# Performance work log

Measured on AMD Instinct MI355X. Metric: run time of the kernel, lower is better.

## Reference

```python
import jax, jax.numpy as jnp
import numpy as np

# Config (matches init_kwargs)
L, B, D, V = 12, 8, 2048, 32000
H, HD, G, N, K = 64, 64, 8, 128, 4
I = H * HD                 # intermediate_size = 4096
CONV = I + 2 * G * N       # conv_dim = 6144
P = I + CONV + H           # in_proj output = 10304
TMAX = 10000.0             # finite replacement for inf time_step_limit


def rmsnorm(x, w, eps=1e-5):
    x32 = x.astype(jnp.float32)
    return (x32 * jax.lax.rsqrt(jnp.mean(x32 * x32, axis=-1, keepdims=True) + eps)) * w


def setup_inputs() -> dict:
    key = jax.random.key(0)
    ks = jax.random.split(key, 10)
    s = 0.02
    return {
        "input_ids": jax.random.randint(ks[0], (B, 1), 0, V),
        "conv_states": jax.random.normal(ks[1], (L, B, CONV, K), dtype=jnp.float32),
        "ssm_states": jax.random.normal(ks[2], (L, B, H, HD, N), dtype=jnp.float32) * 0.1,
        "emb": jax.random.normal(ks[3], (V, D), dtype=jnp.float32) * s,
        "norm_w": jnp.ones((L, D), jnp.float32),
        "in_proj_w": jax.random.normal(ks[4], (L, D, P), dtype=jnp.float32) * s,
        "conv_w": jax.random.normal(ks[5], (L, CONV, K), dtype=jnp.float32) * s,
        "conv_b": jnp.zeros((L, CONV), jnp.float32),
        "dt_bias": jax.random.normal(ks[6], (L, H), dtype=jnp.float32) * s,
        "A_log": jnp.log(jnp.broadcast_to(jnp.arange(1, H + 1, dtype=jnp.float32), (L, H))),
        "D_param": jnp.ones((L, H), jnp.float32),
        "gn_w": jnp.ones((L, I), jnp.float32),
        "out_proj_w": jax.random.normal(ks[7], (L, I, D), dtype=jnp.float32) * s,
        "norm_f_w": jnp.ones((D,), jnp.float32),
        "lm_head_w": jax.random.normal(ks[8], (V, D), dtype=jnp.float32) * s,
    }


def reference(input_ids, conv_states, ssm_states, emb, norm_w, in_proj_w, conv_w,
              conv_b, dt_bias, A_log, D_param, gn_w, out_proj_w, norm_f_w, lm_head_w):
    h = emb[input_ids]  # [B,1,D]

    def layer(h, xs):
        cs, ss, nw, wi, cw, cb, db, al, dp, gw, wo = xs
        residual = h
        hn = rmsnorm(h, nw)                                   # block.norm (RMSNorm)
        proj = jnp.einsum('btd,dp->btp', hn, wi)              # in_proj
        gate, hBC, dt = jnp.split(proj, [I, I + CONV], axis=-1)
        # conv state shift + depthwise conv over kernel dim
        new_in = hBC[:, 0, :]                                 # [B, CONV]
        new_cs = jnp.concatenate([cs[:, :, 1:], new_in[:, :, None]], axis=-1)  # [B,CONV,K]
        conv_out = jnp.sum(new_cs * cw[None], axis=-1) + cb
        conv_out = jax.nn.silu(conv_out)
        x, Bv, Cv = jnp.split(conv_out, [I, I + G * N], axis=-1)
        x = x.reshape(B, H, HD)
        # dt: softplus(dt + dt_bias), clamp to [0, 10000]
        dt_ = jax.nn.softplus(dt[:, 0, :] + db[None, :])       # [B,H]
        dt_ = jnp.clip(dt_, 0.0, TMAX)
        A = -jnp.exp(al)                                       # [H], fp32
        dA = jnp.exp(dt_[:, :, None, None] * A[None, :, None, None])  # [B,H,1,1]
        rep = H // G
        Brep = jnp.repeat(Bv.reshape(B, G, N), rep, axis=1)    # [B,H,N]
        Crep = jnp.repeat(Cv.reshape(B, G, N), rep, axis=1)
        dBx = dt_[:, :, None, None] * Brep[:, :, None, :] * x[:, :, :, None]  # [B,H,HD,N]
        new_ss = ss * dA + dBx
        y = jnp.sum(new_ss * Crep[:, :, None, :], axis=-1)     # [B,H,HD]
        y = y + x * dp[None, :, None]                          # skip via D
        y = y.reshape(B, 1, I)
        # gated RMSNorm: (y * silu(gate)) -> rmsnorm * weight
        yg = y.astype(jnp.float32) * jax.nn.silu(gate.astype(jnp.float32))
        y = rmsnorm(yg, gw)
        out = jnp.einsum('bti,id->btd', y, wo)                 # out_proj
        return residual + out, (new_cs, new_ss)

    h, (new_conv, new_ssm) = jax.lax.scan(
        layer, h,
        (conv_states, ssm_states, norm_w, in_proj_w, conv_w, conv_b,
         dt_bias, A_log, D_param, gn_w, out_proj_w))
    hf = rmsnorm(h, norm_f_w)                                  # norm_f
    logits = jnp.einsum('btd,vd->btv', hf, lm_head_w).astype(jnp.float32)
    return logits, new_conv, new_ssm
```

## Files before the change

### kernel.cpp

```cpp
#include <hip/hip_runtime.h>
#include <hip/hip_bf16.h>
#include <math.h>

#define LNUM 12
#define BNUM 8
#define DNUM 2048
#define VNUM 32000
#define HNUM 64
#define HDNUM 64
#define GNUM 8
#define NNUM 128
#define KNUM 4
#define INUM (HNUM*HDNUM)
#define CONVNUM (INUM + 2*GNUM*NNUM)
#define PNUM (INUM + CONVNUM + HNUM)

#define IP_KC 16
#define GRID 1024

struct MParams {
  const int* ids;
  const float* conv_states; const float* ssm_states;
  const float* emb; const float* norm_w; const float* in_proj_w;
  const float* conv_w; const float* conv_b; const float* dt_bias;
  const float* A_log; const float* D_param; const float* gn_w;
  const float* out_proj_w;
  float* conv_out_st; float* ssm_out_st;
  float* h; float* yg; float* ygsq; float* sqp; float* part1;
  int* arrive;
  int* release;
};

__device__ __forceinline__ float sigmoidf_(float x){ return 1.f/(1.f+expf(-x)); }

__device__ __forceinline__ int   uc_load_i (const int* p){ return __hip_atomic_load((int*)p, __ATOMIC_RELAXED, __HIP_MEMORY_SCOPE_AGENT); }
__device__ __forceinline__ void  uc_store_i(int* p, int v){ __hip_atomic_store(p, v, __ATOMIC_RELAXED, __HIP_MEMORY_SCOPE_AGENT); }
__device__ __forceinline__ float uc_load_f (const float* p){ return __hip_atomic_load((float*)p, __ATOMIC_RELAXED, __HIP_MEMORY_SCOPE_AGENT); }
__device__ __forceinline__ void  uc_store_f(float* p, float v){ __hip_atomic_store(p, v, __ATOMIC_RELAXED, __HIP_MEMORY_SCOPE_AGENT); }
__device__ __forceinline__ void  uc_add_f  (float* p, float v){ __hip_atomic_fetch_add(p, v, __ATOMIC_RELAXED, __HIP_MEMORY_SCOPE_AGENT); }

__device__ __forceinline__ void gbar(const MParams& P, int epoch){
  __syncthreads();
  if (blockIdx.x == 0){
    for (int i = 1 + threadIdx.x; i < GRID; i += 256){
      long spins = 0;
      while (uc_load_i(&P.arrive[i*16]) < epoch){
        __builtin_amdgcn_s_sleep(1);
        if (++spins > (1L<<22)) break;
      }
    }
    __syncthreads();
    if (threadIdx.x == 0){
      asm volatile("s_waitcnt vmcnt(0) lgkmcnt(0)" ::: "memory");
      uc_store_i(P.release, epoch);
    }
  } else {
    if (threadIdx.x == 0){
      asm volatile("s_waitcnt vmcnt(0) lgkmcnt(0)" ::: "memory");
      uc_store_i(&P.arrive[blockIdx.x*16], epoch);
      long spins = 0;
      while (uc_load_i(P.release) < epoch){
        __builtin_amdgcn_s_sleep(1);
        if (++spins > (1L<<22)) break;
      }
    }
    __syncthreads();
  }
  asm volatile("" ::: "memory");
}

__global__ __launch_bounds__(256, 4) void k_mamba(MParams P){
  const int blk = blockIdx.x, t = threadIdx.x;
  const int w = t >> 6, l = t & 63;
  __shared__ float smem[3088];
  int bar_no = 0;

  if (blk < BNUM){
    int b = blk;
    const float* src = P.emb + (size_t)P.ids[b]*DNUM;
    float* dst = P.h + (size_t)b*DNUM;
    float4 v0 = *(const float4*)(src + t*4);
    float4 v1 = *(const float4*)(src + 1024 + t*4);
    uc_store_f(dst + t*4 + 0, v0.x); uc_store_f(dst + t*4 + 1, v0.y);
    uc_store_f(dst + t*4 + 2, v0.z); uc_store_f(dst + t*4 + 3, v0.w);
    uc_store_f(dst + 1024 + t*4 + 0, v1.x); uc_store_f(dst + 1024 + t*4 + 1, v1.y);
    uc_store_f(dst + 1024 + t*4 + 2, v1.z); uc_store_f(dst + 1024 + t*4 + 3, v1.w);
    float q = v0.x*v0.x+v0.y*v0.y+v0.z*v0.z+v0.w*v0.w
            + v1.x*v1.x+v1.y*v1.y+v1.z*v1.z+v1.w*v1.w;
    q += __shfl_xor(q,32); q += __shfl_xor(q,16); q += __shfl_xor(q,8);
    q += __shfl_xor(q,4);  q += __shfl_xor(q,2);  q += __shfl_xor(q,1);
    if (l == 0) smem[w] = q;
    __syncthreads();
    if (t == 0) uc_store_f(&P.sqp[b], smem[0]+smem[1]+smem[2]+smem[3]);
  }
  gbar(P, ++bar_no);

  for (int li = 0; li < LNUM; ++li){
    const float* Wi   = P.in_proj_w  + (size_t)li*DNUM*PNUM;
    const float* nw   = P.norm_w     + (size_t)li*DNUM;
    const float* cw   = P.conv_w     + (size_t)li*CONVNUM*KNUM;
    const float* cb   = P.conv_b     + (size_t)li*CONVNUM;
    const float* db   = P.dt_bias    + (size_t)li*HNUM;
    const float* al   = P.A_log      + (size_t)li*HNUM;
    const float* dpp  = P.D_param    + (size_t)li*HNUM;
    const float* gw   = P.gn_w       + (size_t)li*INUM;
    const float* Wo   = P.out_proj_w + (size_t)li*INUM*DNUM;
    const float* csin = P.conv_states + (size_t)li*BNUM*CONVNUM*KNUM;
    float*       csout= P.conv_out_st + (size_t)li*BNUM*CONVNUM*KNUM;
    const float* ssin = P.ssm_states  + (size_t)li*BNUM*HNUM*HDNUM*NNUM;
    float*       ssout= P.ssm_out_st  + (size_t)li*BNUM*HNUM*HDNUM*NNUM;

    {
      float*  xs  = smem;
      float4* red = (float4*)(smem + 1024);
      if (blk < 896){
        int pb = blk % 56, kc = blk / 56;
        int r0 = kc*128;
        for (int i = t; i < BNUM*128; i += 256){
          int b = i>>7, dl = i&127;
          xs[i] = uc_load_f(&P.h[b*DNUM + r0 + dl]) * nw[r0 + dl];
        }
        __syncthreads();
        int p0 = pb*256 + l*4;
        bool valid = (p0 < PNUM);
        float4 acc[BNUM];
        #pragma unroll
        for (int b = 0; b < BNUM; ++b) acc[b] = make_float4(0.f,0.f,0.f,0.f);
        if (valid){
          int rbase = w*32;
          const float* wp = Wi + (size_t)(r0 + rbase)*PNUM + p0;
          #pragma unroll 4
          for (int r = 0; r < 32; ++r){
            float4 w4 = *(const float4*)wp;
            wp += PNUM;
            #pragma unroll
            for (int b = 0; b < BNUM; ++b){
              float xvv = xs[b*128 + rbase + r];
              acc[b].x += xvv*w4.x; acc[b].y += xvv*w4.y; acc[b].z += xvv*w4.z; acc[b].w += xvv*w4.w;
            }
          }
        }
        #pragma unroll
        for (int rw = 1; rw < 4; ++rw){
          if (w == rw){
            #pragma unroll
            for (int b = 0; b < BNUM; ++b) red[b*64 + l] = acc[b];
          }
          __syncthreads();
          if (w == 0){
            #pragma unroll
            for (int b = 0; b < BNUM; ++b){
              float4 r4 = red[b*64 + l];
              acc[b].x += r4.x; acc[b].y += r4.y; acc[b].z += r4.z; acc[b].w += r4.w;
            }
          }
          __syncthreads();
        }
        if (w == 0){
          #pragma unroll
          for (int b = 0; b < BNUM; ++b) red[b*64 + l] = acc[b];
        }
        __syncthreads();
        const float* redf = (const float*)red;
        if (pb*256 + t < PNUM){
          #pragma unroll
          for (int b = 0; b < BNUM; ++b)
            uc_store_f(&P.part1[(size_t)(kc*BNUM + b)*PNUM + pb*256 + t], redf[b*256 + t]);
        }
      } else if (blk < 896 + BNUM){
        int b = blk - 896;
        float q = 0.f;
        for (int i = t; i < DNUM; i += 256){
          float v = uc_load_f(&P.h[b*DNUM + i]);
          q += v*v;
        }
        q += __shfl_xor(q,32); q += __shfl_xor(q,16); q += __shfl_xor(q,8);
        q += __shfl_xor(q,4);  q += __shfl_xor(q,2);  q += __shfl_xor(q,1);
        if (l == 0) smem[w] = q;
        __syncthreads();
        if (t == 0) uc_store_f(&P.sqp[b], smem[0]+smem[1]+smem[2]+smem[3]);
      }
    }
    gbar(P, ++bar_no);

    {
      float* xv    = smem;
      float* gatel = smem + 32;
      float* Bsh   = smem + 64;
      float* Csh   = smem + 192;
      float* scal  = smem + 320;
      float* sred  = smem + 328;
      int b = blk >> 7, rest = blk & 127, hh = rest >> 1, half = rest & 1, g = hh >> 3;
      if (t == 0) scal[2] = rsqrtf(uc_load_f(&P.sqp[b]) * (1.f/DNUM) + 1e-5f);
      __syncthreads();
      float inv = scal[2];
      {
        int n = t & 127;
        int c = (t < 128) ? (INUM + g*NNUM + n) : (INUM + GNUM*NNUM + g*NNUM + n);
        int p = INUM + c;
        float v = 0.f;
        #pragma unroll
        for (int kc2 = 0; kc2 < IP_KC; ++kc2) v += uc_load_f(&P.part1[(size_t)(kc2*BNUM + b)*PNUM + p]);
        v *= inv;
        size_t sid = (size_t)b*CONVNUM + c;
        float4 s4 = *(const float4*)(csin + sid*KNUM);
        float4 ns = make_float4(s4.y, s4.z, s4.w, v);
        if ((hh & 7) == 0 && half == 0) *(float4*)(csout + sid*KNUM) = ns;
        float4 w4 = *(const float4*)(cw + (size_t)c*KNUM);
        float co = ns.x*w4.x + ns.y*w4.y + ns.z*w4.z + ns.w*w4.w + cb[c];
        float sv = co * sigmoidf_(co);
        if (t < 128) Bsh[n] = sv; else Csh[n] = sv;
      }
      if (t < 32){
        int hd = half*32 + t;
        int c = hh*HDNUM + hd;
        int p = INUM + c;
        float v = 0.f;
        #pragma unroll
        for (int kc2 = 0; kc2 < IP_KC; ++kc2) v += uc_load_f(&P.part1[(size_t)(kc2*BNUM + b)*PNUM + p]);
        v *= inv;
        size_t sid = (size_t)b*CONVNUM + c;
        float4 s4 = *(const float4*)(csin + sid*KNUM);
        float4 ns = make_float4(s4.y, s4.z, s4.w, v);
        *(float4*)(csout + sid*KNUM) = ns;
        float4 w4 = *(const float4*)(cw + (size_t)c*KNUM);
        float co = ns.x*w4.x + ns.y*w4.y + ns.z*w4.z + ns.w*w4.w + cb[c];
        xv[t] = co * sigmoidf_(co);
      } else if (t < 64){
        int hd = half*32 + (t-32);
        int p = hh*HDNUM + hd;
        float v = 0.f;
        #pragma unroll
        for (int kc2 = 0; kc2 < IP_KC; ++kc2) v += uc_load_f(&P.part1[(size_t)(kc2*BNUM + b)*PNUM + p]);
        gatel[t-32] = v * inv;
      } else if (t == 64){
        int p = INUM + CONVNUM + hh;
        float v = 0.f;
        #pragma unroll
        for (int kc2 = 0; kc2 < IP_KC; ++kc2) v += uc_load_f(&P.part1[(size_t)(kc2*BNUM + b)*PNUM + p]);
        float dtr = v*inv + db[hh];
        float dt = (dtr > 20.f) ? dtr : log1pf(expf(dtr));
        dt = fminf(dt, 10000.f);
        scal[0] = dt;
        scal[1] = expf(dt * (-expf(al[hh])));
      }
      __syncthreads();
      float dt = scal[0], dA = scal[1], dp = dpp[hh];
      int r = t & 31, a2 = t >> 5;
      float4 Bv = *(float4*)&Bsh[r*4];
      float4 Cv = *(float4*)&Csh[r*4];
      const float* si = ssin  + (size_t)(b*HNUM + hh)*HDNUM*NNUM + half*4096;
      float*       so = ssout + (size_t)(b*HNUM + hh)*HDNUM*NNUM + half*4096;
      float s_yg = 0.f;
      #pragma unroll
      for (int k = 0; k < 4; ++k){
        int hdl = k*8 + a2;
        float xvv = xv[hdl];
        float coef = dt * xvv;
        int off = k*1024 + t*4;
        float4 s4 = *(const float4*)(si + off);
        float4 ns;
        ns.x = s4.x*dA + coef*Bv.x;
        ns.y = s4.y*dA + coef*Bv.y;
        ns.z = s4.z*dA + coef*Bv.z;
        ns.w = s4.w*dA + coef*Bv.w;
        *(float4*)(so + off) = ns;
        float yp = ns.x*Cv.x + ns.y*Cv.y + ns.z*Cv.z + ns.w*Cv.w;
        yp += __shfl_xor(yp,1); yp += __shfl_xor(yp,2); yp += __shfl_xor(yp,4);
        yp += __shfl_xor(yp,8); yp += __shfl_xor(yp,16);
        if (r == 0){
          float gv = gatel[hdl];
          float ygv = (yp + xvv*dp) * gv * sigmoidf_(gv);
          uc_store_f(&P.yg[b*INUM + hh*HDNUM + half*32 + hdl], ygv);
          s_yg += ygv*ygv;
        }
      }
      if (r == 0) sred[a2] = s_yg;
      __syncthreads();
      if (t == 0){
        float tot = 0.f;
        #pragma unroll
        for (int j = 0; j < 8; ++j) tot += sred[j];
        uc_store_f(&P.ygsq[b*128 + hh*2 + half], tot);
      }
    }
    gbar(P, ++bar_no);

    {
      float*  xs   = smem;
      float*  invg = smem + 512;
      float2* red2 = (float2*)(smem + 528);
      int pb = blk & 15, kc = blk >> 4;
      if (t < 64){
        int b2 = t>>3, j = t&7;
        float v = 0.f;
        #pragma unroll
        for (int jj = 0; jj < 16; ++jj) v += uc_load_f(&P.ygsq[b2*128 + j + jj*8]);
        v += __shfl_xor(v,1); v += __shfl_xor(v,2); v += __shfl_xor(v,4);
        if (j == 0) invg[b2] = rsqrtf(v*(1.f/INUM) + 1e-5f);
      }
      __syncthreads();
      int r0 = kc*64;
      for (int i = t; i < BNUM*64; i += 256){
        int b = i>>6, il = i&63;
        xs[i] = uc_load_f(&P.yg[b*INUM + r0 + il]) * invg[b] * gw[r0 + il];
      }
      __syncthreads();
      int c0 = pb*128 + l*2;
      float2 acc[BNUM];
      #pragma unroll
      for (int b = 0; b < BNUM; ++b) acc[b] = make_float2(0.f,0.f);
      {
        int rbase = w*16;
        const float* wp = Wo + (size_t)(r0 + rbase)*DNUM + c0;
        #pragma unroll 4
        for (int r2 = 0; r2 < 16; ++r2){
          float2 w2 = *(const float2*)wp;
          wp += DNUM;
          #pragma unroll
          for (int b = 0; b < BNUM; ++b){
            float xvv = xs[b*64 + rbase + r2];
            acc[b].x += xvv*w2.x; acc[b].y += xvv*w2.y;
          }
        }
      }
      #pragma unroll
      for (int rw = 1; rw < 4; ++rw){
        if (w == rw){
          #pragma unroll
          for (int b = 0; b < BNUM; ++b) red2[b*64 + l] = acc[b];
        }
        __syncthreads();
        if (w == 0){
          #pragma unroll
          for (int b = 0; b < BNUM; ++b){
            float2 r2v = red2[b*64 + l];
            acc[b].x += r2v.x; acc[b].y += r2v.y;
          }
        }
        __syncthreads();
      }
      if (w == 0){
        #pragma unroll
        for (int b = 0; b < BNUM; ++b) red2[b*64 + l] = acc[b];
      }
      __syncthreads();
      const float* redf = (const float*)red2;
      #pragma unroll
      for (int bb = 0; bb < 4; ++bb){
        int b = bb*2 + (t>>7);
        int cc = t & 127;
        uc_add_f(&P.h[b*DNUM + pb*128 + cc], redf[b*128 + cc]);
      }
    }
    gbar(P, ++bar_no);
  }

  if (blk >= 896 && blk < 896 + BNUM){
    int b = blk - 896;
    float q = 0.f;
    for (int i = t; i < DNUM; i += 256){
      float v = uc_load_f(&P.h[b*DNUM + i]);
      q += v*v;
    }
    q += __shfl_xor(q,32); q += __shfl_xor(q,16); q += __shfl_xor(q,8);
    q += __shfl_xor(q,4);  q += __shfl_xor(q,2);  q += __shfl_xor(q,1);
    if (l == 0) smem[w] = q;
    __syncthreads();
    if (t == 0) uc_store_f(&P.sqp[b], smem[0]+smem[1]+smem[2]+smem[3]);
  }
}

__global__ __launch_bounds__(256) void k_lmhead(const float* __restrict__ h,
                                                const float* __restrict__ sqp,
                                                const float* __restrict__ nf,
                                                const float* __restrict__ Wl,
                                                float* __restrict__ logits){
  __shared__ float hs[BNUM*DNUM];
  __shared__ float invb_s[8];
  int t = threadIdx.x;
  if (t < 8) invb_s[t] = rsqrtf(sqp[t]*(1.f/DNUM) + 1e-5f);
  __syncthreads();
  #pragma unroll
  for (int it = 0; it < 16; ++it){
    int i = t*4 + it*1024;
    float iv = invb_s[it>>1];
    float4 hv  = *(const float4*)(h + i);
    float4 nfv = *(const float4*)(nf + (i & 2047));
    float4 o;
    o.x = hv.x*iv*nfv.x; o.y = hv.y*iv*nfv.y; o.z = hv.z*iv*nfv.z; o.w = hv.w*iv*nfv.w;
    *(float4*)(hs + i) = o;
  }
  __syncthreads();
  int wv = t >> 6, lane = t & 63;
  int v0 = (blockIdx.x*4 + wv)*4;
  float acc[4][BNUM];
  #pragma unroll
  for (int u = 0; u < 4; ++u)
    #pragma unroll
    for (int b = 0; b < BNUM; ++b) acc[u][b] = 0.f;
  #pragma unroll
  for (int j = 0; j < 8; ++j){
    int dbase = j*256 + lane*4;
    float4 w0 = *(const float4*)(Wl + (size_t)(v0+0)*DNUM + dbase);
    float4 w1 = *(const float4*)(Wl + (size_t)(v0+1)*DNUM + dbase);
    float4 w2 = *(const float4*)(Wl + (size_t)(v0+2)*DNUM + dbase);
    float4 w3 = *(const float4*)(Wl + (size_t)(v0+3)*DNUM + dbase);
    #pragma unroll
    for (int b = 0; b < BNUM; ++b){
      float4 hv = *(const float4*)(hs + b*DNUM + dbase);
      acc[0][b] += w0.x*hv.x + w0.y*hv.y + w0.z*hv.z + w0.w*hv.w;
      acc[1][b] += w1.x*hv.x + w1.y*hv.y + w1.z*hv.z + w1.w*hv.w;
      acc[2][b] += w2.x*hv.x + w2.y*hv.y + w2.z*hv.z + w2.w*hv.w;
      acc[3][b] += w3.x*hv.x + w3.y*hv.y + w3.z*hv.z + w3.w*hv.w;
    }
  }
  #pragma unroll
  for (int u = 0; u < 4; ++u)
    #pragma unroll
    for (int b = 0; b < BNUM; ++b){
      float s = acc[u][b];
      s += __shfl_xor(s,32); s += __shfl_xor(s,16); s += __shfl_xor(s,8);
      s += __shfl_xor(s,4);  s += __shfl_xor(s,2);  s += __shfl_xor(s,1);
      if (lane == 0) logits[(size_t)b*VNUM + v0 + u] = s;
    }
}

extern "C" void kernel_launch(void* const* d_in, const int* in_sizes, int n_in,
                              void* d_out, int out_size, void* d_ws, size_t ws_size,
                              hipStream_t stream){
  const int*   ids         = (const int*)d_in[0];
  const float* conv_states = (const float*)d_in[1];
  const float* ssm_states  = (const float*)d_in[2];
  const float* emb         = (const float*)d_in[3];
  const float* norm_w      = (const float*)d_in[4];
  const float* in_proj_w   = (const float*)d_in[5];
  const float* conv_w      = (const float*)d_in[6];
  const float* conv_b      = (const float*)d_in[7];
  const float* dt_bias     = (const float*)d_in[8];
  const float* A_log       = (const float*)d_in[9];
  const float* D_param     = (const float*)d_in[10];
  const float* gn_w        = (const float*)d_in[11];
  const float* out_proj_w  = (const float*)d_in[12];
  const float* norm_f_w    = (const float*)d_in[13];
  const float* lm_head_w   = (const float*)d_in[14];

  float* out         = (float*)d_out;
  float* logits      = out;
  float* conv_out_st = out + (size_t)BNUM*VNUM;
  float* ssm_out_st  = conv_out_st + (size_t)LNUM*BNUM*CONVNUM*KNUM;

  float* ws    = (float*)d_ws;
  float* h     = ws;
  float* yg    = h    + 16384;
  float* ygsq  = yg   + 32768;
  float* sqp   = ygsq + 1024;
  float* part1 = sqp  + 64;
  int*   bar   = (int*)(part1 + 1830912);

  hipMemsetAsync(bar, 0, (GRID*16 + 16)*sizeof(int), stream);

  MParams P;
  P.ids = ids; P.conv_states = conv_states; P.ssm_states = ssm_states;
  P.emb = emb; P.norm_w = norm_w; P.in_proj_w = in_proj_w;
  P.conv_w = conv_w; P.conv_b = conv_b; P.dt_bias = dt_bias;
  P.A_log = A_log; P.D_param = D_param; P.gn_w = gn_w;
  P.out_proj_w = out_proj_w;
  P.conv_out_st = conv_out_st; P.ssm_out_st = ssm_out_st;
  P.h = h; P.yg = yg; P.ygsq = ygsq; P.sqp = sqp; P.part1 = part1;
  P.arrive = bar; P.release = bar + GRID*16;

  k_mamba<<<GRID, 256, 0, stream>>>(P);
  k_lmhead<<<VNUM/16, 256, 0, stream>>>(h, sqp, norm_f_w, lm_head_w, logits);
}
```

Baseline: 1.155 ms.

## Replace global barriers with per-stage dataflow counters and retile out_proj

Replaces the centralized grid barrier with per-stage counter flags. The SSM stage now waits only on the in_proj column strips and the norm partial it needs, and out_proj waits on grouped completion counters. The in_proj grid is trimmed to 41 strips × 16 K-chunks. out_proj is retiled to 512-row K-chunks with 16-column strips and a different shared-memory reduction. The aim is to cut barrier latency and idle time between stages, at the cost of more flag traffic, larger shared memory, and correctness that depends on the flag counts and timeouts.

Result: slower. 1.381 ms (+19.5%).

```diff
diff --git a/kernel.cpp b/kernel.cpp
--- a/kernel.cpp
+++ b/kernel.cpp
@@ -16,6 +16,8 @@
 #define PNUM (INUM + CONVNUM + HNUM)
 
 #define IP_KC 16
+#define NSTRIP 41
+#define A_TILES (NSTRIP*IP_KC)
 #define GRID 1024
 
 struct MParams {
@@ -27,53 +29,59 @@
   const float* out_proj_w;
   float* conv_out_st; float* ssm_out_st;
   float* h; float* yg; float* ygsq; float* sqp; float* part1;
-  int* arrive;
-  int* release;
+  int* flagE; int* flagS; int* flagA; int* flagC; int* flagD;
 };
 
 __device__ __forceinline__ float sigmoidf_(float x){ return 1.f/(1.f+expf(-x)); }
 
 __device__ __forceinline__ int   uc_load_i (const int* p){ return __hip_atomic_load((int*)p, __ATOMIC_RELAXED, __HIP_MEMORY_SCOPE_AGENT); }
-__device__ __forceinline__ void  uc_store_i(int* p, int v){ __hip_atomic_store(p, v, __ATOMIC_RELAXED, __HIP_MEMORY_SCOPE_AGENT); }
 __device__ __forceinline__ float uc_load_f (const float* p){ return __hip_atomic_load((float*)p, __ATOMIC_RELAXED, __HIP_MEMORY_SCOPE_AGENT); }
 __device__ __forceinline__ void  uc_store_f(float* p, float v){ __hip_atomic_store(p, v, __ATOMIC_RELAXED, __HIP_MEMORY_SCOPE_AGENT); }
 __device__ __forceinline__ void  uc_add_f  (float* p, float v){ __hip_atomic_fetch_add(p, v, __ATOMIC_RELAXED, __HIP_MEMORY_SCOPE_AGENT); }
-
-__device__ __forceinline__ void gbar(const MParams& P, int epoch){
+__device__ __forceinline__ void  uc_inc_i  (int* p){ __hip_atomic_fetch_add(p, 1, __ATOMIC_RELAXED, __HIP_MEMORY_SCOPE_AGENT); }
+
+__device__ __forceinline__ void flag_inc(int* line){
   __syncthreads();
-  if (blockIdx.x == 0){
-    for (int i = 1 + threadIdx.x; i < GRID; i += 256){
-      long spins = 0;
-      while (uc_load_i(&P.arrive[i*16]) < epoch){
-        __builtin_amdgcn_s_sleep(1);
-        if (++spins > (1L<<22)) break;
-      }
+  if (threadIdx.x == 0){
+    asm volatile("s_waitcnt vmcnt(0) lgkmcnt(0)" ::: "memory");
+    uc_inc_i(line);
+  }
+}
+
+__device__ __forceinline__ void wait_line(const int* line, int target){
+  if (threadIdx.x == 0){
+    long sp = 0;
+    while (uc_load_i(line) < target){
+      __builtin_amdgcn_s_sleep(4);
+      if (++sp > (1L<<19)) break;
+    }
+  }
+  __syncthreads();
+}
+
+__device__ __forceinline__ void wait_grp(const int* grp, int target){
+  __shared__ int done_s;
+  if (threadIdx.x == 0) done_s = 0;
+  __syncthreads();
+  long sp = 0;
+  for (;;){
+    if (threadIdx.x < 64){
+      int v = (threadIdx.x < 32) ? uc_load_i(&grp[threadIdx.x*16]) : 0;
+      v += __shfl_xor(v,1); v += __shfl_xor(v,2); v += __shfl_xor(v,4);
+      v += __shfl_xor(v,8); v += __shfl_xor(v,16); v += __shfl_xor(v,32);
+      if (threadIdx.x == 0) done_s = (v >= target);
     }
     __syncthreads();
-    if (threadIdx.x == 0){
-      asm volatile("s_waitcnt vmcnt(0) lgkmcnt(0)" ::: "memory");
-      uc_store_i(P.release, epoch);
-    }
-  } else {
-    if (threadIdx.x == 0){
-      asm volatile("s_waitcnt vmcnt(0) lgkmcnt(0)" ::: "memory");
-      uc_store_i(&P.arrive[blockIdx.x*16], epoch);
-      long spins = 0;
-      while (uc_load_i(P.release) < epoch){
-        __builtin_amdgcn_s_sleep(1);
-        if (++spins > (1L<<22)) break;
-      }
-    }
+    if (done_s || ++sp > (1L<<18)) break;
+    __builtin_amdgcn_s_sleep(4);
     __syncthreads();
   }
-  asm volatile("" ::: "memory");
 }
 
 __global__ __launch_bounds__(256, 4) void k_mamba(MParams P){
   const int blk = blockIdx.x, t = threadIdx.x;
   const int w = t >> 6, l = t & 63;
-  __shared__ float smem[3088];
-  int bar_no = 0;
+  __shared__ float smem[8256];
 
   if (blk < BNUM){
     int b = blk;
@@ -85,15 +93,8 @@
     uc_store_f(dst + t*4 + 2, v0.z); uc_store_f(dst + t*4 + 3, v0.w);
     uc_store_f(dst + 1024 + t*4 + 0, v1.x); uc_store_f(dst + 1024 + t*4 + 1, v1.y);
     uc_store_f(dst + 1024 + t*4 + 2, v1.z); uc_store_f(dst + 1024 + t*4 + 3, v1.w);
-    float q = v0.x*v0.x+v0.y*v0.y+v0.z*v0.z+v0.w*v0.w
-            + v1.x*v1.x+v1.y*v1.y+v1.z*v1.z+v1.w*v1.w;
-    q += __shfl_xor(q,32); q += __shfl_xor(q,16); q += __shfl_xor(q,8);
-    q += __shfl_xor(q,4);  q += __shfl_xor(q,2);  q += __shfl_xor(q,1);
-    if (l == 0) smem[w] = q;
-    __syncthreads();
-    if (t == 0) uc_store_f(&P.sqp[b], smem[0]+smem[1]+smem[2]+smem[3]);
-  }
-  gbar(P, ++bar_no);
+    flag_inc(P.flagE);
+  }
 
   for (int li = 0; li < LNUM; ++li){
     const float* Wi   = P.in_proj_w  + (size_t)li*DNUM*PNUM;
@@ -110,87 +111,111 @@
     const float* ssin = P.ssm_states  + (size_t)li*BNUM*HNUM*HDNUM*NNUM;
     float*       ssout= P.ssm_out_st  + (size_t)li*BNUM*HNUM*HDNUM*NNUM;
 
-    {
+    if (li == 0) wait_line(P.flagE, BNUM);
+    else         wait_grp(P.flagD + (li-1)*512, GRID);
+
+    if (blk < A_TILES){
       float*  xs  = smem;
-      float4* red = (float4*)(smem + 1024);
-      if (blk < 896){
-        int pb = blk % 56, kc = blk / 56;
-        int r0 = kc*128;
-        for (int i = t; i < BNUM*128; i += 256){
-          int b = i>>7, dl = i&127;
-          xs[i] = uc_load_f(&P.h[b*DNUM + r0 + dl]) * nw[r0 + dl];
+      float4* red = (float4*)(smem + 1040);
+      int pb = blk % NSTRIP, kc = blk / NSTRIP;
+      int r0 = kc*128;
+      for (int i = t; i < BNUM*128; i += 256){
+        int b = i>>7, dl = i&127;
+        xs[i] = uc_load_f(&P.h[b*DNUM + r0 + dl]) * nw[r0 + dl];
+      }
+      __syncthreads();
+      int p0 = pb*256 + l*4;
+      bool valid = (p0 < PNUM);
+      float4 acc[BNUM];
+      #pragma unroll
+      for (int b = 0; b < BNUM; ++b) acc[b] = make_float4(0.f,0.f,0.f,0.f);
+      if (valid){
+        int rbase = w*32;
+        const float* wp = Wi + (size_t)(r0 + rbase)*PNUM + p0;
+        #pragma unroll 4
+        for (int r = 0; r < 32; ++r){
+          float4 w4 = *(const float4*)wp;
+          wp += PNUM;
+          #pragma unroll
+          for (int b = 0; b < BNUM; ++b){
+            float xvv = xs[b*128 + rbase + r];
+            acc[b].x += xvv*w4.x; acc[b].y += xvv*w4.y; acc[b].z += xvv*w4.z; acc[b].w += xvv*w4.w;
+          }
+        }
+      }
+      #pragma unroll
+      for (int rw = 1; rw < 4; ++rw){
+        if (w == rw){
+          #pragma unroll
+          for (int b = 0; b < BNUM; ++b) red[b*64 + l] = acc[b];
         }
         __syncthreads();
-        int p0 = pb*256 + l*4;
-        bool valid = (p0 < PNUM);
-        float4 acc[BNUM];
-        #pragma unroll
-        for (int b = 0; b < BNUM; ++b) acc[b] = make_float4(0.f,0.f,0.f,0.f);
-        if (valid){
-          int rbase = w*32;
-          const float* wp = Wi + (size_t)(r0 + rbase)*PNUM + p0;
-          #pragma unroll 4
-          for (int r = 0; r < 32; ++r){
-            float4 w4 = *(const float4*)wp;
-            wp += PNUM;
-            #pragma unroll
-            for (int b = 0; b < BNUM; ++b){
-              float xvv = xs[b*128 + rbase + r];
-              acc[b].x += xvv*w4.x; acc[b].y += xvv*w4.y; acc[b].z += xvv*w4.z; acc[b].w += xvv*w4.w;
-            }
-          }
-        }
-        #pragma unroll
-        for (int rw = 1; rw < 4; ++rw){
-          if (w == rw){
-            #pragma unroll
-            for (int b = 0; b < BNUM; ++b) red[b*64 + l] = acc[b];
-          }
-          __syncthreads();
-          if (w == 0){
-            #pragma unroll
-            for (int b = 0; b < BNUM; ++b){
-              float4 r4 = red[b*64 + l];
-              acc[b].x += r4.x; acc[b].y += r4.y; acc[b].z += r4.z; acc[b].w += r4.w;
-            }
-          }
-          __syncthreads();
-        }
         if (w == 0){
           #pragma unroll
-          for (int b = 0; b < BNUM; ++b) red[b*64 + l] = acc[b];
+          for (int b = 0; b < BNUM; ++b){
+            float4 r4 = red[b*64 + l];
+            acc[b].x += r4.x; acc[b].y += r4.y; acc[b].z += r4.z; acc[b].w += r4.w;
+          }
         }
         __syncthreads();
-        const float* redf = (const float*)red;
-        if (pb*256 + t < PNUM){
-          #pragma unroll
-          for (int b = 0; b < BNUM; ++b)
-            uc_store_f(&P.part1[(size_t)(kc*BNUM + b)*PNUM + pb*256 + t], redf[b*256 + t]);
-        }
-      } else if (blk < 896 + BNUM){
-        int b = blk - 896;
-        float q = 0.f;
-        for (int i = t; i < DNUM; i += 256){
-          float v = uc_load_f(&P.h[b*DNUM + i]);
-          q += v*v;
-        }
-        q += __shfl_xor(q,32); q += __shfl_xor(q,16); q += __shfl_xor(q,8);
-        q += __shfl_xor(q,4);  q += __shfl_xor(q,2);  q += __shfl_xor(q,1);
-        if (l == 0) smem[w] = q;
+      }
+      if (w == 0){
+        #pragma unroll
+        for (int b = 0; b < BNUM; ++b) red[b*64 + l] = acc[b];
+      }
+      __syncthreads();
+      const float* redf = (const float*)red;
+      if (pb*256 + t < PNUM){
+        #pragma unroll
+        for (int b = 0; b < BNUM; ++b)
+          uc_store_f(&P.part1[(size_t)(kc*BNUM + b)*PNUM + pb*256 + t], redf[b*256 + t]);
+      }
+      flag_inc(&P.flagA[li*896 + pb*16]);
+    } else if (blk < A_TILES + BNUM){
+      int b = blk - A_TILES;
+      float q = 0.f;
+      for (int i = t; i < DNUM; i += 256){
+        float v = uc_load_f(&P.h[b*DNUM + i]);
+        q += v*v;
+      }
+      q += __shfl_xor(q,32); q += __shfl_xor(q,16); q += __shfl_xor(q,8);
+      q += __shfl_xor(q,4);  q += __shfl_xor(q,2);  q += __shfl_xor(q,1);
+      if (l == 0) smem[w] = q;
+      __syncthreads();
+      if (t == 0) uc_store_f(&P.sqp[b], smem[0]+smem[1]+smem[2]+smem[3]);
+      flag_inc(&P.flagS[li*16]);
+    }
+
+    {
+      int b = blk >> 7, rest = blk & 127, hh = rest >> 1, half = rest & 1, g = hh >> 3;
+      {
+        int s_g = (hh*HDNUM + half*32) >> 8;
+        int s_x = (INUM + hh*HDNUM + half*32) >> 8;
+        int s_B = (2*INUM + g*NNUM) >> 8;
+        int s_C = (2*INUM + GNUM*NNUM + g*NNUM) >> 8;
+        int s_dt = (INUM + CONVNUM) >> 8;
+        const int* line = nullptr; int tgt = IP_KC;
+        if      (t == 0) line = &P.flagA[li*896 + s_g*16];
+        else if (t == 1) line = &P.flagA[li*896 + s_x*16];
+        else if (t == 2) line = &P.flagA[li*896 + s_B*16];
+        else if (t == 3) line = &P.flagA[li*896 + s_C*16];
+        else if (t == 4) line = &P.flagA[li*896 + s_dt*16];
+        else if (t == 5){ line = &P.flagS[li*16]; tgt = BNUM; }
+        if (line){
+          long sp = 0;
+          while (uc_load_i(line) < tgt){
+            __builtin_amdgcn_s_sleep(4);
+            if (++sp > (1L<<19)) break;
+          }
+        }
         __syncthreads();
-        if (t == 0) uc_store_f(&P.sqp[b], smem[0]+smem[1]+smem[2]+smem[3]);
-      }
-    }
-    gbar(P, ++bar_no);
-
-    {
+      }
       float* xv    = smem;
       float* gatel = smem + 32;
       float* Bsh   = smem + 64;
       float* Csh   = smem + 192;
       float* scal  = smem + 320;
       float* sred  = smem + 328;
-      int b = blk >> 7, rest = blk & 127, hh = rest >> 1, half = rest & 1, g = hh >> 3;
       if (t == 0) scal[2] = rsqrtf(uc_load_f(&P.sqp[b]) * (1.f/DNUM) + 1e-5f);
       __syncthreads();
       float inv = scal[2];
@@ -283,14 +308,16 @@
         for (int j = 0; j < 8; ++j) tot += sred[j];
         uc_store_f(&P.ygsq[b*128 + hh*2 + half], tot);
       }
-    }
-    gbar(P, ++bar_no);
+      flag_inc(&P.flagC[li*512 + (blk>>5)*16]);
+    }
 
     {
+      wait_grp(P.flagC + li*512, GRID);
       float*  xs   = smem;
-      float*  invg = smem + 512;
-      float2* red2 = (float2*)(smem + 528);
-      int pb = blk & 15, kc = blk >> 4;
+      float*  invg = smem + 4096;
+      float2* red2 = (float2*)(smem + 4112);
+      int pb = blk & 127, kc = blk >> 7;
+      int c0 = pb*16, r0 = kc*512;
       if (t < 64){
         int b2 = t>>3, j = t&7;
         float v = 0.f;
@@ -300,64 +327,48 @@
         if (j == 0) invg[b2] = rsqrtf(v*(1.f/INUM) + 1e-5f);
       }
       __syncthreads();
-      int r0 = kc*64;
-      for (int i = t; i < BNUM*64; i += 256){
-        int b = i>>6, il = i&63;
+      for (int i = t; i < BNUM*512; i += 256){
+        int b = i>>9, il = i&511;
         xs[i] = uc_load_f(&P.yg[b*INUM + r0 + il]) * invg[b] * gw[r0 + il];
       }
       __syncthreads();
-      int c0 = pb*128 + l*2;
-      float2 acc[BNUM];
+      int cp = t & 7, rg = t >> 3;
+      float2 acc2[BNUM];
       #pragma unroll
-      for (int b = 0; b < BNUM; ++b) acc[b] = make_float2(0.f,0.f);
-      {
-        int rbase = w*16;
-        const float* wp = Wo + (size_t)(r0 + rbase)*DNUM + c0;
-        #pragma unroll 4
-        for (int r2 = 0; r2 < 16; ++r2){
-          float2 w2 = *(const float2*)wp;
-          wp += DNUM;
-          #pragma unroll
-          for (int b = 0; b < BNUM; ++b){
-            float xvv = xs[b*64 + rbase + r2];
-            acc[b].x += xvv*w2.x; acc[b].y += xvv*w2.y;
-          }
+      for (int b = 0; b < BNUM; ++b) acc2[b] = make_float2(0.f,0.f);
+      const float* wp = Wo + (size_t)(r0 + rg)*DNUM + c0 + cp*2;
+      #pragma unroll 4
+      for (int it = 0; it < 16; ++it){
+        float2 w2 = *(const float2*)wp;
+        wp += (size_t)32*DNUM;
+        int rr = rg + it*32;
+        #pragma unroll
+        for (int b = 0; b < BNUM; ++b){
+          float xvv = xs[b*512 + rr];
+          acc2[b].x += xvv*w2.x; acc2[b].y += xvv*w2.y;
         }
       }
       #pragma unroll
-      for (int rw = 1; rw < 4; ++rw){
-        if (w == rw){
-          #pragma unroll
-          for (int b = 0; b < BNUM; ++b) red2[b*64 + l] = acc[b];
-        }
-        __syncthreads();
-        if (w == 0){
-          #pragma unroll
-          for (int b = 0; b < BNUM; ++b){
-            float2 r2v = red2[b*64 + l];
-            acc[b].x += r2v.x; acc[b].y += r2v.y;
-          }
-        }
-        __syncthreads();
-      }
-      if (w == 0){
-        #pragma unroll
-        for (int b = 0; b < BNUM; ++b) red2[b*64 + l] = acc[b];
-      }
-      __syncthreads();
-      const float* redf = (const float*)red2;
-      #pragma unroll
-      for (int bb = 0; bb < 4; ++bb){
-        int b = bb*2 + (t>>7);
-        int cc = t & 127;
-        uc_add_f(&P.h[b*DNUM + pb*128 + cc], redf[b*128 + cc]);
-      }
-    }
-    gbar(P, ++bar_no);
-  }
-
-  if (blk >= 896 && blk < 896 + BNUM){
-    int b = blk - 896;
+      for (int b = 0; b < BNUM; ++b) red2[(rg*8 + cp)*8 + b] = acc2[b];
+      __syncthreads();
+      if (t < 64){
+        int cpi = t & 7, b = t >> 3;
+        float sx = 0.f, sy = 0.f;
+        #pragma unroll 8
+        for (int rgi = 0; rgi < 32; ++rgi){
+          float2 v2 = red2[(rgi*8 + cpi)*8 + b];
+          sx += v2.x; sy += v2.y;
+        }
+        uc_add_f(&P.h[b*DNUM + c0 + cpi*2 + 0], sx);
+        uc_add_f(&P.h[b*DNUM + c0 + cpi*2 + 1], sy);
+      }
+      flag_inc(&P.flagD[li*512 + (blk>>5)*16]);
+    }
+  }
+
+  if (blk >= A_TILES && blk < A_TILES + BNUM){
+    wait_grp(P.flagD + (LNUM-1)*512, GRID);
+    int b = blk - A_TILES;
     float q = 0.f;
     for (int i = t; i < DNUM; i += 256){
       float v = uc_load_f(&P.h[b*DNUM + i]);
@@ -456,9 +467,15 @@
   float* ygsq  = yg   + 32768;
   float* sqp   = ygsq + 1024;
   float* part1 = sqp  + 64;
-  int*   bar   = (int*)(part1 + 1830912);
-
-  hipMemsetAsync(bar, 0, (GRID*16 + 16)*sizeof(int), stream);
+  int*   bar   = (int*)(part1 + 1318912);
+
+  int* flagE = bar;
+  int* flagS = flagE + 16;
+  int* flagA = flagS + 12*16;
+  int* flagC = flagA + 12*56*16;
+  int* flagD = flagC + 12*32*16;
+  size_t flag_bytes = (size_t)(16 + 12*16 + 12*56*16 + 12*32*16 + 12*32*16) * sizeof(int);
+  hipMemsetAsync(bar, 0, flag_bytes, stream);
 
   MParams P;
   P.ids = ids; P.conv_states = conv_states; P.ssm_states = ssm_states;
@@ -468,7 +485,7 @@
   P.out_proj_w = out_proj_w;
   P.conv_out_st = conv_out_st; P.ssm_out_st = ssm_out_st;
   P.h = h; P.yg = yg; P.ygsq = ygsq; P.sqp = sqp; P.part1 = part1;
-  P.arrive = bar; P.release = bar + GRID*16;
+  P.flagE = flagE; P.flagS = flagS; P.flagA = flagA; P.flagC = flagC; P.flagD = flagD;
 
   k_mamba<<<GRID, 256, 0, stream>>>(P);
   k_lmhead<<<VNUM/16, 256, 0, stream>>>(h, sqp, norm_f_w, lm_head_w, logits);
```

## Replace per-phase grid barriers with fine-grained dataflow flags and deferred residual

Applied to the files above, without the earlier changes.

Three of the four grid-wide barriers per layer are replaced with per-strip, per-head and zeroing counters. Consumer blocks poll only the producer tiles they depend on. The out_proj partials now accumulate into a delta buffer, and the gated-RMSNorm scale is folded into the next layer's in_proj input (h_prev + inv*delta) using double-buffered h/delta/ygsq. This removes the separate gated-norm inverse pass before out_proj and lets stages overlap. The in_proj tiling shrinks to 41 strips x 16 k-chunks so the grid tiles are assigned exactly, and unroll factors are raised. The cost is more flag traffic, polling with bounded spins, and more complex correctness ordering.

New measurement: 1.165 ms. About the same (+0.8%).

```diff
diff --git a/kernel.cpp b/kernel.cpp
--- a/kernel.cpp
+++ b/kernel.cpp
@@ -16,6 +16,8 @@
 #define PNUM (INUM + CONVNUM + HNUM)
 
 #define IP_KC 16
+#define NSTRIP 41
+#define A_TILES (NSTRIP*IP_KC)
 #define GRID 1024
 
 struct MParams {
@@ -26,9 +28,10 @@
   const float* A_log; const float* D_param; const float* gn_w;
   const float* out_proj_w;
   float* conv_out_st; float* ssm_out_st;
-  float* h; float* yg; float* ygsq; float* sqp; float* part1;
-  int* arrive;
-  int* release;
+  float* hb0; float* hb1; float* dl0; float* dl1; float* hf;
+  float* yg; float* ygsq; float* sqp; float* part1;
+  int* arrive; int* release;
+  int* flagE; int* flagS; int* flagA; int* flagC; int* flagZ;
 };
 
 __device__ __forceinline__ float sigmoidf_(float x){ return 1.f/(1.f+expf(-x)); }
@@ -38,15 +41,36 @@
 __device__ __forceinline__ float uc_load_f (const float* p){ return __hip_atomic_load((float*)p, __ATOMIC_RELAXED, __HIP_MEMORY_SCOPE_AGENT); }
 __device__ __forceinline__ void  uc_store_f(float* p, float v){ __hip_atomic_store(p, v, __ATOMIC_RELAXED, __HIP_MEMORY_SCOPE_AGENT); }
 __device__ __forceinline__ void  uc_add_f  (float* p, float v){ __hip_atomic_fetch_add(p, v, __ATOMIC_RELAXED, __HIP_MEMORY_SCOPE_AGENT); }
+__device__ __forceinline__ void  uc_inc_i  (int* p){ __hip_atomic_fetch_add(p, 1, __ATOMIC_RELAXED, __HIP_MEMORY_SCOPE_AGENT); }
+
+__device__ __forceinline__ void flag_inc(int* line){
+  __syncthreads();
+  if (threadIdx.x == 0){
+    asm volatile("s_waitcnt vmcnt(0) lgkmcnt(0)" ::: "memory");
+    uc_inc_i(line);
+  }
+}
+
+__device__ __forceinline__ void poll_line(const int* line, int target){
+  long sp = 0;
+  while (uc_load_i(line) < target){
+    __builtin_amdgcn_s_sleep(4);
+    if (++sp > (1L<<20)) break;
+  }
+}
+__device__ __forceinline__ void wait_line(const int* line, int target){
+  if (threadIdx.x == 0) poll_line(line, target);
+  __syncthreads();
+}
 
 __device__ __forceinline__ void gbar(const MParams& P, int epoch){
   __syncthreads();
   if (blockIdx.x == 0){
     for (int i = 1 + threadIdx.x; i < GRID; i += 256){
-      long spins = 0;
+      long sp = 0;
       while (uc_load_i(&P.arrive[i*16]) < epoch){
         __builtin_amdgcn_s_sleep(1);
-        if (++spins > (1L<<22)) break;
+        if (++sp > (1L<<22)) break;
       }
     }
     __syncthreads();
@@ -58,10 +82,10 @@
     if (threadIdx.x == 0){
       asm volatile("s_waitcnt vmcnt(0) lgkmcnt(0)" ::: "memory");
       uc_store_i(&P.arrive[blockIdx.x*16], epoch);
-      long spins = 0;
+      long sp = 0;
       while (uc_load_i(P.release) < epoch){
         __builtin_amdgcn_s_sleep(1);
-        if (++spins > (1L<<22)) break;
+        if (++sp > (1L<<22)) break;
       }
     }
     __syncthreads();
@@ -73,27 +97,20 @@
   const int blk = blockIdx.x, t = threadIdx.x;
   const int w = t >> 6, l = t & 63;
   __shared__ float smem[3088];
-  int bar_no = 0;
+  int ep = 0;
 
   if (blk < BNUM){
     int b = blk;
     const float* src = P.emb + (size_t)P.ids[b]*DNUM;
-    float* dst = P.h + (size_t)b*DNUM;
+    float* dst = P.hb0 + (size_t)b*DNUM;
     float4 v0 = *(const float4*)(src + t*4);
     float4 v1 = *(const float4*)(src + 1024 + t*4);
     uc_store_f(dst + t*4 + 0, v0.x); uc_store_f(dst + t*4 + 1, v0.y);
     uc_store_f(dst + t*4 + 2, v0.z); uc_store_f(dst + t*4 + 3, v0.w);
     uc_store_f(dst + 1024 + t*4 + 0, v1.x); uc_store_f(dst + 1024 + t*4 + 1, v1.y);
     uc_store_f(dst + 1024 + t*4 + 2, v1.z); uc_store_f(dst + 1024 + t*4 + 3, v1.w);
-    float q = v0.x*v0.x+v0.y*v0.y+v0.z*v0.z+v0.w*v0.w
-            + v1.x*v1.x+v1.y*v1.y+v1.z*v1.z+v1.w*v1.w;
-    q += __shfl_xor(q,32); q += __shfl_xor(q,16); q += __shfl_xor(q,8);
-    q += __shfl_xor(q,4);  q += __shfl_xor(q,2);  q += __shfl_xor(q,1);
-    if (l == 0) smem[w] = q;
-    __syncthreads();
-    if (t == 0) uc_store_f(&P.sqp[b], smem[0]+smem[1]+smem[2]+smem[3]);
-  }
-  gbar(P, ++bar_no);
+    flag_inc(P.flagE);
+  }
 
   for (int li = 0; li < LNUM; ++li){
     const float* Wi   = P.in_proj_w  + (size_t)li*DNUM*PNUM;
@@ -110,87 +127,149 @@
     const float* ssin = P.ssm_states  + (size_t)li*BNUM*HNUM*HDNUM*NNUM;
     float*       ssout= P.ssm_out_st  + (size_t)li*BNUM*HNUM*HDNUM*NNUM;
 
-    {
-      float*  xs  = smem;
-      float4* red = (float4*)(smem + 1024);
-      if (blk < 896){
-        int pb = blk % 56, kc = blk / 56;
-        int r0 = kc*128;
+    float* hbase = ((li-1)&1) ? P.hb1 : P.hb0;
+    float* hwrite= (li&1) ? P.hb1 : P.hb0;
+    float* dprev = ((li-1)&1) ? P.dl1 : P.dl0;
+    float* dcur  = (li&1) ? P.dl1 : P.dl0;
+    const float* ygsq_prev = P.ygsq + (((li-1)&1) ? 1024 : 0);
+    float*       ygsq_cur  = P.ygsq + ((li&1) ? 1024 : 0);
+    if (li == 0) hbase = P.hb0;
+
+    if (li == 0) wait_line(P.flagE, BNUM);
+    else         gbar(P, ++ep);
+
+    if (blk < A_TILES){
+      float*  xs   = smem;
+      float*  invs = smem + 1024;
+      float4* red  = (float4*)(smem + 1040);
+      int pb = blk % NSTRIP, kc = blk / NSTRIP;
+      int r0 = kc*128;
+      if (li > 0){
+        if (t < 64){
+          int b2 = t>>3, j = t&7;
+          float v = 0.f;
+          #pragma unroll
+          for (int jj = 0; jj < 16; ++jj) v += uc_load_f(&ygsq_prev[b2*128 + j + jj*8]);
+          v += __shfl_xor(v,1); v += __shfl_xor(v,2); v += __shfl_xor(v,4);
+          if (j == 0) invs[b2] = rsqrtf(v*(1.f/INUM) + 1e-5f);
+        }
+        __syncthreads();
         for (int i = t; i < BNUM*128; i += 256){
           int b = i>>7, dl = i&127;
-          xs[i] = uc_load_f(&P.h[b*DNUM + r0 + dl]) * nw[r0 + dl];
-        }
-        __syncthreads();
-        int p0 = pb*256 + l*4;
-        bool valid = (p0 < PNUM);
-        float4 acc[BNUM];
-        #pragma unroll
-        for (int b = 0; b < BNUM; ++b) acc[b] = make_float4(0.f,0.f,0.f,0.f);
-        if (valid){
-          int rbase = w*32;
-          const float* wp = Wi + (size_t)(r0 + rbase)*PNUM + p0;
-          #pragma unroll 4
-          for (int r = 0; r < 32; ++r){
-            float4 w4 = *(const float4*)wp;
-            wp += PNUM;
-            #pragma unroll
-            for (int b = 0; b < BNUM; ++b){
-              float xvv = xs[b*128 + rbase + r];
-              acc[b].x += xvv*w4.x; acc[b].y += xvv*w4.y; acc[b].z += xvv*w4.z; acc[b].w += xvv*w4.w;
-            }
+          float hv = uc_load_f(&hbase[b*DNUM + r0 + dl]) + invs[b]*uc_load_f(&dprev[b*DNUM + r0 + dl]);
+          xs[i] = hv * nw[r0 + dl];
+        }
+      } else {
+        for (int i = t; i < BNUM*128; i += 256){
+          int b = i>>7, dl = i&127;
+          xs[i] = uc_load_f(&hbase[b*DNUM + r0 + dl]) * nw[r0 + dl];
+        }
+      }
+      __syncthreads();
+      int p0 = pb*256 + l*4;
+      bool valid = (p0 < PNUM);
+      float4 acc[BNUM];
+      #pragma unroll
+      for (int b = 0; b < BNUM; ++b) acc[b] = make_float4(0.f,0.f,0.f,0.f);
+      if (valid){
+        int rbase = w*32;
+        const float* wp = Wi + (size_t)(r0 + rbase)*PNUM + p0;
+        #pragma unroll 8
+        for (int r = 0; r < 32; ++r){
+          float4 w4 = *(const float4*)wp;
+          wp += PNUM;
+          #pragma unroll
+          for (int b = 0; b < BNUM; ++b){
+            float xvv = xs[b*128 + rbase + r];
+            acc[b].x += xvv*w4.x; acc[b].y += xvv*w4.y; acc[b].z += xvv*w4.z; acc[b].w += xvv*w4.w;
           }
         }
-        #pragma unroll
-        for (int rw = 1; rw < 4; ++rw){
-          if (w == rw){
-            #pragma unroll
-            for (int b = 0; b < BNUM; ++b) red[b*64 + l] = acc[b];
+      }
+      #pragma unroll
+      for (int rw = 1; rw < 4; ++rw){
+        if (w == rw){
+          #pragma unroll
+          for (int b = 0; b < BNUM; ++b) red[b*64 + l] = acc[b];
+        }
+        __syncthreads();
+        if (w == 0){
+          #pragma unroll
+          for (int b = 0; b < BNUM; ++b){
+            float4 r4 = red[b*64 + l];
+            acc[b].x += r4.x; acc[b].y += r4.y; acc[b].z += r4.z; acc[b].w += r4.w;
           }
-          __syncthreads();
-          if (w == 0){
-            #pragma unroll
-            for (int b = 0; b < BNUM; ++b){
-              float4 r4 = red[b*64 + l];
-              acc[b].x += r4.x; acc[b].y += r4.y; acc[b].z += r4.z; acc[b].w += r4.w;
-            }
-          }
-          __syncthreads();
-        }
-        if (w == 0){
-          #pragma unroll
-          for (int b = 0; b < BNUM; ++b) red[b*64 + l] = acc[b];
-        }
-        __syncthreads();
-        const float* redf = (const float*)red;
-        if (pb*256 + t < PNUM){
-          #pragma unroll
-          for (int b = 0; b < BNUM; ++b)
-            uc_store_f(&P.part1[(size_t)(kc*BNUM + b)*PNUM + pb*256 + t], redf[b*256 + t]);
-        }
-      } else if (blk < 896 + BNUM){
-        int b = blk - 896;
-        float q = 0.f;
-        for (int i = t; i < DNUM; i += 256){
-          float v = uc_load_f(&P.h[b*DNUM + i]);
-          q += v*v;
-        }
-        q += __shfl_xor(q,32); q += __shfl_xor(q,16); q += __shfl_xor(q,8);
-        q += __shfl_xor(q,4);  q += __shfl_xor(q,2);  q += __shfl_xor(q,1);
-        if (l == 0) smem[w] = q;
-        __syncthreads();
-        if (t == 0) uc_store_f(&P.sqp[b], smem[0]+smem[1]+smem[2]+smem[3]);
-      }
-    }
-    gbar(P, ++bar_no);
+        }
+        __syncthreads();
+      }
+      if (w == 0){
+        #pragma unroll
+        for (int b = 0; b < BNUM; ++b) red[b*64 + l] = acc[b];
+      }
+      __syncthreads();
+      const float* redf = (const float*)red;
+      if (pb*256 + t < PNUM){
+        #pragma unroll
+        for (int b = 0; b < BNUM; ++b)
+          uc_store_f(&P.part1[(size_t)(kc*BNUM + b)*PNUM + pb*256 + t], redf[b*256 + t]);
+      }
+      flag_inc(&P.flagA[(li*NSTRIP + pb)*16]);
+    } else if (blk < A_TILES + BNUM){
+      int b = blk - A_TILES;
+      float ivg = 0.f;
+      if (li > 0){
+        float v = (t < 128) ? uc_load_f(&ygsq_prev[b*128 + t]) : 0.f;
+        v += __shfl_xor(v,1); v += __shfl_xor(v,2); v += __shfl_xor(v,4);
+        v += __shfl_xor(v,8); v += __shfl_xor(v,16); v += __shfl_xor(v,32);
+        if (l == 0) smem[w] = v;
+        __syncthreads();
+        ivg = rsqrtf((smem[0]+smem[1]+smem[2]+smem[3])*(1.f/INUM) + 1e-5f);
+        __syncthreads();
+      }
+      float q = 0.f;
+      for (int i = t; i < DNUM; i += 256){
+        float hv;
+        if (li > 0){
+          hv = uc_load_f(&hbase[b*DNUM + i]) + ivg*uc_load_f(&dprev[b*DNUM + i]);
+          uc_store_f(&hwrite[b*DNUM + i], hv);
+        } else {
+          hv = uc_load_f(&hbase[b*DNUM + i]);
+        }
+        q += hv*hv;
+      }
+      q += __shfl_xor(q,32); q += __shfl_xor(q,16); q += __shfl_xor(q,8);
+      q += __shfl_xor(q,4);  q += __shfl_xor(q,2);  q += __shfl_xor(q,1);
+      if (l == 0) smem[4+w] = q;
+      __syncthreads();
+      if (t == 0) uc_store_f(&P.sqp[b], smem[4]+smem[5]+smem[6]+smem[7]);
+      flag_inc(&P.flagS[li*16]);
+    } else if (blk < A_TILES + BNUM + 16){
+      int z = blk - A_TILES - BNUM;
+      for (int i = t; i < 1024; i += 256) uc_store_f(&dcur[z*1024 + i], 0.f);
+      flag_inc(&P.flagZ[li*16]);
+    }
 
     {
+      int b = blk >> 7, rest = blk & 127, hh = rest >> 1, half = rest & 1, g = hh >> 3;
+      {
+        int s_g  = (hh*HDNUM + half*32) >> 8;
+        int s_x  = (INUM + hh*HDNUM + half*32) >> 8;
+        int s_B  = (2*INUM + g*NNUM) >> 8;
+        int s_C  = (2*INUM + GNUM*NNUM + g*NNUM) >> 8;
+        int s_dt = (INUM + CONVNUM) >> 8;
+        if      (t == 0) poll_line(&P.flagA[(li*NSTRIP + s_g)*16], IP_KC);
+        else if (t == 1) poll_line(&P.flagA[(li*NSTRIP + s_x)*16], IP_KC);
+        else if (t == 2) poll_line(&P.flagA[(li*NSTRIP + s_B)*16], IP_KC);
+        else if (t == 3) poll_line(&P.flagA[(li*NSTRIP + s_C)*16], IP_KC);
+        else if (t == 4) poll_line(&P.flagA[(li*NSTRIP + s_dt)*16], IP_KC);
+        else if (t == 5) poll_line(&P.flagS[li*16], BNUM);
+        __syncthreads();
+      }
       float* xv    = smem;
       float* gatel = smem + 32;
       float* Bsh   = smem + 64;
       float* Csh   = smem + 192;
       float* scal  = smem + 320;
       float* sred  = smem + 328;
-      int b = blk >> 7, rest = blk & 127, hh = rest >> 1, half = rest & 1, g = hh >> 3;
       if (t == 0) scal[2] = rsqrtf(uc_load_f(&P.sqp[b]) * (1.f/DNUM) + 1e-5f);
       __syncthreads();
       float inv = scal[2];
@@ -281,29 +360,22 @@
         float tot = 0.f;
         #pragma unroll
         for (int j = 0; j < 8; ++j) tot += sred[j];
-        uc_store_f(&P.ygsq[b*128 + hh*2 + half], tot);
-      }
-    }
-    gbar(P, ++bar_no);
+        uc_store_f(&ygsq_cur[b*128 + hh*2 + half], tot);
+      }
+      flag_inc(&P.flagC[(li*HNUM + hh)*16]);
+    }
 
     {
+      int pb = blk & 15, kc = blk >> 4;
+      if      (t == 0) poll_line(&P.flagC[(li*HNUM + kc)*16], 16);
+      else if (t == 1) poll_line(&P.flagZ[li*16], 16);
+      __syncthreads();
       float*  xs   = smem;
-      float*  invg = smem + 512;
       float2* red2 = (float2*)(smem + 528);
-      int pb = blk & 15, kc = blk >> 4;
-      if (t < 64){
-        int b2 = t>>3, j = t&7;
-        float v = 0.f;
-        #pragma unroll
-        for (int jj = 0; jj < 16; ++jj) v += uc_load_f(&P.ygsq[b2*128 + j + jj*8]);
-        v += __shfl_xor(v,1); v += __shfl_xor(v,2); v += __shfl_xor(v,4);
-        if (j == 0) invg[b2] = rsqrtf(v*(1.f/INUM) + 1e-5f);
-      }
-      __syncthreads();
       int r0 = kc*64;
       for (int i = t; i < BNUM*64; i += 256){
         int b = i>>6, il = i&63;
-        xs[i] = uc_load_f(&P.yg[b*INUM + r0 + il]) * invg[b] * gw[r0 + il];
+        xs[i] = uc_load_f(&P.yg[b*INUM + r0 + il]) * gw[r0 + il];
       }
       __syncthreads();
       int c0 = pb*128 + l*2;
@@ -313,7 +385,7 @@
       {
         int rbase = w*16;
         const float* wp = Wo + (size_t)(r0 + rbase)*DNUM + c0;
-        #pragma unroll 4
+        #pragma unroll 8
         for (int r2 = 0; r2 < 16; ++r2){
           float2 w2 = *(const float2*)wp;
           wp += DNUM;
@@ -350,28 +422,37 @@
       for (int bb = 0; bb < 4; ++bb){
         int b = bb*2 + (t>>7);
         int cc = t & 127;
-        uc_add_f(&P.h[b*DNUM + pb*128 + cc], redf[b*128 + cc]);
-      }
-    }
-    gbar(P, ++bar_no);
-  }
-
-  if (blk >= 896 && blk < 896 + BNUM){
-    int b = blk - 896;
+        uc_add_f(&dcur[b*DNUM + pb*128 + cc], redf[b*128 + cc]);
+      }
+    }
+  }
+
+  gbar(P, ++ep);
+  if (blk >= A_TILES && blk < A_TILES + BNUM){
+    int b = blk - A_TILES;
+    const float* ygsq_last = P.ygsq + 1024;
+    float v = (t < 128) ? uc_load_f(&ygsq_last[b*128 + t]) : 0.f;
+    v += __shfl_xor(v,1); v += __shfl_xor(v,2); v += __shfl_xor(v,4);
+    v += __shfl_xor(v,8); v += __shfl_xor(v,16); v += __shfl_xor(v,32);
+    if (l == 0) smem[w] = v;
+    __syncthreads();
+    float ivg = rsqrtf((smem[0]+smem[1]+smem[2]+smem[3])*(1.f/INUM) + 1e-5f);
+    __syncthreads();
     float q = 0.f;
     for (int i = t; i < DNUM; i += 256){
-      float v = uc_load_f(&P.h[b*DNUM + i]);
-      q += v*v;
+      float hv = uc_load_f(&P.hb1[b*DNUM + i]) + ivg*uc_load_f(&P.dl1[b*DNUM + i]);
+      P.hf[b*DNUM + i] = hv;
+      q += hv*hv;
     }
     q += __shfl_xor(q,32); q += __shfl_xor(q,16); q += __shfl_xor(q,8);
     q += __shfl_xor(q,4);  q += __shfl_xor(q,2);  q += __shfl_xor(q,1);
-    if (l == 0) smem[w] = q;
+    if (l == 0) smem[4+w] = q;
     __syncthreads();
-    if (t == 0) uc_store_f(&P.sqp[b], smem[0]+smem[1]+smem[2]+smem[3]);
-  }
-}
-
-__global__ __launch_bounds__(256) void k_lmhead(const float* __restrict__ h,
+    if (t == 0) P.sqp[b] = smem[4]+smem[5]+smem[6]+smem[7];
+  }
+}
+
+__global__ __launch_bounds__(256) void k_lmhead(const float* __restrict__ hf,
                                                 const float* __restrict__ sqp,
                                                 const float* __restrict__ nf,
                                                 const float* __restrict__ Wl,
@@ -385,7 +466,7 @@
   for (int it = 0; it < 16; ++it){
     int i = t*4 + it*1024;
     float iv = invb_s[it>>1];
-    float4 hv  = *(const float4*)(h + i);
+    float4 hv  = *(const float4*)(hf + i);
     float4 nfv = *(const float4*)(nf + (i & 2047));
     float4 o;
     o.x = hv.x*iv*nfv.x; o.y = hv.y*iv*nfv.y; o.z = hv.z*iv*nfv.z; o.w = hv.w*iv*nfv.w;
@@ -451,14 +532,26 @@
   float* ssm_out_st  = conv_out_st + (size_t)LNUM*BNUM*CONVNUM*KNUM;
 
   float* ws    = (float*)d_ws;
-  float* h     = ws;
-  float* yg    = h    + 16384;
+  float* hb0   = ws;
+  float* hb1   = hb0  + 16384;
+  float* dl0   = hb1  + 16384;
+  float* dl1   = dl0  + 16384;
+  float* hf    = dl1  + 16384;
+  float* yg    = hf   + 16384;
   float* ygsq  = yg   + 32768;
-  float* sqp   = ygsq + 1024;
+  float* sqp   = ygsq + 2048;
   float* part1 = sqp  + 64;
-  int*   bar   = (int*)(part1 + 1830912);
-
-  hipMemsetAsync(bar, 0, (GRID*16 + 16)*sizeof(int), stream);
+  int*   bar   = (int*)(part1 + 1318912);
+
+  int* arrive = bar;
+  int* release= arrive + GRID*16;
+  int* flagE  = release + 16;
+  int* flagS  = flagE + 16;
+  int* flagA  = flagS + 12*16;
+  int* flagC  = flagA + 12*NSTRIP*16;
+  int* flagZ  = flagC + 12*HNUM*16;
+  size_t flag_ints = (size_t)(GRID*16 + 16 + 16 + 12*16 + 12*NSTRIP*16 + 12*HNUM*16 + 12*16);
+  hipMemsetAsync(bar, 0, flag_ints*sizeof(int), stream);
 
   MParams P;
   P.ids = ids; P.conv_states = conv_states; P.ssm_states = ssm_states;
@@ -467,9 +560,11 @@
   P.A_log = A_log; P.D_param = D_param; P.gn_w = gn_w;
   P.out_proj_w = out_proj_w;
   P.conv_out_st = conv_out_st; P.ssm_out_st = ssm_out_st;
-  P.h = h; P.yg = yg; P.ygsq = ygsq; P.sqp = sqp; P.part1 = part1;
-  P.arrive = bar; P.release = bar + GRID*16;
+  P.hb0 = hb0; P.hb1 = hb1; P.dl0 = dl0; P.dl1 = dl1; P.hf = hf;
+  P.yg = yg; P.ygsq = ygsq; P.sqp = sqp; P.part1 = part1;
+  P.arrive = arrive; P.release = release;
+  P.flagE = flagE; P.flagS = flagS; P.flagA = flagA; P.flagC = flagC; P.flagZ = flagZ;
 
   k_mamba<<<GRID, 256, 0, stream>>>(P);
-  k_lmhead<<<VNUM/16, 256, 0, stream>>>(h, sqp, norm_f_w, lm_head_w, logits);
-}
+  k_lmhead<<<VNUM/16, 256, 0, stream>>>(hf, sqp, norm_f_w, lm_head_w, logits);
+}
```
